# Kernel tuning notes

Hardware: AMD Instinct MI355X
Metric: run time of the kernel (lower is better)

## Reference

```python
import jax, jax.numpy as jnp
import numpy as np


def setup_inputs() -> dict:
    key = jax.random.key(0)
    k1, k2 = jax.random.split(key)
    N, D, K = 1048576, 128, 262144
    data = jax.random.normal(k1, (N, D), dtype=jnp.float32)
    # unique in-range indices (index depth 1 -> scatter rows of data)
    indices = jnp.arange(K, dtype=jnp.int64).reshape(K, 1)
    updates = jax.random.normal(k2, (K, D), dtype=jnp.float32)
    return {"data": data, "indices": indices, "updates": updates}


def reference(data, indices, updates):
    # ScatterND with reduction=1 (add): out = clone(data); out[idx] += updates
    # indices: [K, 1] -> row indices [K]; updates: [K, D]
    idx = indices[..., 0].astype(jnp.int32)
    # indices are unique, so .at[].add matches torch's gather-add-scatter exactly
    return data.at[idx].add(updates)
```

## Files before the change

### kernel.cpp

```cpp
#include <hip/hip_runtime.h>


__global__ void inv_init_kernel(int4* __restrict__ inv4, int n4) {
    int i = blockIdx.x * blockDim.x + threadIdx.x;
    if (i < n4) inv4[i] = make_int4(-1, -1, -1, -1);
}

__global__ void inv_scatter_kernel(const int* __restrict__ idx,
                                   int* __restrict__ inv, int K) {
    int k = blockIdx.x * blockDim.x + threadIdx.x;
    if (k < K) inv[idx[k]] = k;
}

__global__ void fused_scatter_add_kernel(const float4* __restrict__ data,
                                         const float4* __restrict__ upd,
                                         const int* __restrict__ inv,
                                         float4* __restrict__ out,
                                         int nvec, unsigned dvec) {
    int i = blockIdx.x * blockDim.x + threadIdx.x;
    if (i >= nvec) return;
    unsigned row  = (unsigned)i / dvec;
    unsigned lane = (unsigned)i - row * dvec;
    float4 v = data[i];
    int k = inv[row];
    if (k >= 0) {
        float4 u = upd[(long long)k * dvec + lane];
        v.x += u.x; v.y += u.y; v.z += u.z; v.w += u.w;
    }
    out[i] = v;
}

__global__ void copy_kernel(const float4* __restrict__ src,
                            float4* __restrict__ dst, int nvec) {
    int i = blockIdx.x * blockDim.x + threadIdx.x;
    if (i < nvec) dst[i] = src[i];
}

__global__ void rmw_add_kernel(const float4* __restrict__ upd,
                               const int* __restrict__ idx,
                               float4* __restrict__ out,
                               int kvec, unsigned dvec) {
    int i = blockIdx.x * blockDim.x + threadIdx.x;
    if (i >= kvec) return;
    unsigned k    = (unsigned)i / dvec;
    unsigned lane = (unsigned)i - k * dvec;
    long long off = (long long)idx[k] * dvec + lane;
    float4 u = upd[i];
    float4 v = out[off];
    v.x += u.x; v.y += u.y; v.z += u.z; v.w += u.w;
    out[off] = v;
}

extern "C" void kernel_launch(void* const* d_in, const int* in_sizes, int n_in,
                              void* d_out, int out_size, void* d_ws, size_t ws_size,
                              hipStream_t stream) {
    const float* data = (const float*)d_in[0];
    const int*   idx  = (const int*)d_in[1];
    const float* upd  = (const float*)d_in[2];
    float* out = (float*)d_out;

    const int K = in_sizes[1];
    const int D = in_sizes[2] / K;
    const int N = in_sizes[0] / D;
    const unsigned dvec = (unsigned)(D / 4);
    const int nvec = in_sizes[0] / 4;
    const int kvec = in_sizes[2] / 4;

    const int BS = 256;

    if (ws_size >= (size_t)N * sizeof(int)) {
        int* inv = (int*)d_ws;
        int n4 = N / 4;
        inv_init_kernel<<<(n4 + BS - 1) / BS, BS, 0, stream>>>((int4*)inv, n4);
        inv_scatter_kernel<<<(K + BS - 1) / BS, BS, 0, stream>>>(idx, inv, K);
        fused_scatter_add_kernel<<<(nvec + BS - 1) / BS, BS, 0, stream>>>(
            (const float4*)data, (const float4*)upd, inv, (float4*)out, nvec, dvec);
    } else {
        copy_kernel<<<(nvec + BS - 1) / BS, BS, 0, stream>>>(
            (const float4*)data, (float4*)out, nvec);
        rmw_add_kernel<<<(kvec + BS - 1) / BS, BS, 0, stream>>>(
            (const float4*)upd, idx, (float4*)out, kvec, dvec);
    }
}
```

Baseline: 894.4 us.

## Store inverse index map in output tail and use shift/mask indexing

The inverse row map now lives in the last rows of the output buffer instead of the workspace, so the fused gather-add path runs even when no workspace is provided. The fused kernel covers every row except those tail rows. The tail rows are then copied from the input, and a per-index kernel applies any updates that target them. Row and lane indexing use shift and mask when the vector width is a power of two. The change removes the fallback copy plus read-modify-write passes but adds two small extra launches and relies on the map being consumed before the tail is overwritten.

Result: no change. 898.3 us (+0.4%).

```diff
diff --git a/kernel.cpp b/kernel.cpp
--- a/kernel.cpp
+++ b/kernel.cpp
@@ -16,9 +16,28 @@
                                          const float4* __restrict__ upd,
                                          const int* __restrict__ inv,
                                          float4* __restrict__ out,
-                                         int nvec, unsigned dvec) {
+                                         int nvec_main, unsigned shift,
+                                         unsigned lanemask) {
     int i = blockIdx.x * blockDim.x + threadIdx.x;
-    if (i >= nvec) return;
+    if (i >= nvec_main) return;
+    unsigned row  = (unsigned)i >> shift;
+    unsigned lane = (unsigned)i & lanemask;
+    float4 v = data[i];
+    int k = inv[row];
+    if (k >= 0) {
+        float4 u = upd[((long long)k << shift) + lane];
+        v.x += u.x; v.y += u.y; v.z += u.z; v.w += u.w;
+    }
+    out[i] = v;
+}
+
+__global__ void fused_scatter_add_div_kernel(const float4* __restrict__ data,
+                                             const float4* __restrict__ upd,
+                                             const int* __restrict__ inv,
+                                             float4* __restrict__ out,
+                                             int nvec_main, unsigned dvec) {
+    int i = blockIdx.x * blockDim.x + threadIdx.x;
+    if (i >= nvec_main) return;
     unsigned row  = (unsigned)i / dvec;
     unsigned lane = (unsigned)i - row * dvec;
     float4 v = data[i];
@@ -36,19 +55,22 @@
     if (i < nvec) dst[i] = src[i];
 }
 
-__global__ void rmw_add_kernel(const float4* __restrict__ upd,
-                               const int* __restrict__ idx,
-                               float4* __restrict__ out,
-                               int kvec, unsigned dvec) {
-    int i = blockIdx.x * blockDim.x + threadIdx.x;
-    if (i >= kvec) return;
-    unsigned k    = (unsigned)i / dvec;
-    unsigned lane = (unsigned)i - k * dvec;
-    long long off = (long long)idx[k] * dvec + lane;
-    float4 u = upd[i];
-    float4 v = out[off];
-    v.x += u.x; v.y += u.y; v.z += u.z; v.w += u.w;
-    out[off] = v;
+__global__ void tail_rmw_kernel(const float4* __restrict__ upd,
+                                const int* __restrict__ idx,
+                                float4* __restrict__ out,
+                                int K, int row_lo, unsigned dvec) {
+    int k = blockIdx.x * blockDim.x + threadIdx.x;
+    if (k >= K) return;
+    int r = idx[k];
+    if (r < row_lo) return;
+    const float4* u = upd + (long long)k * dvec;
+    float4*       o = out + (long long)r * dvec;
+    for (unsigned j = 0; j < dvec; ++j) {
+        float4 v = o[j];
+        float4 uu = u[j];
+        v.x += uu.x; v.y += uu.y; v.z += uu.z; v.w += uu.w;
+        o[j] = v;
+    }
 }
 
 extern "C" void kernel_launch(void* const* d_in, const int* in_sizes, int n_in,
@@ -63,22 +85,38 @@
     const int D = in_sizes[2] / K;
     const int N = in_sizes[0] / D;
     const unsigned dvec = (unsigned)(D / 4);
-    const int nvec = in_sizes[0] / 4;
-    const int kvec = in_sizes[2] / 4;
 
     const int BS = 256;
 
-    if (ws_size >= (size_t)N * sizeof(int)) {
-        int* inv = (int*)d_ws;
-        int n4 = N / 4;
-        inv_init_kernel<<<(n4 + BS - 1) / BS, BS, 0, stream>>>((int4*)inv, n4);
-        inv_scatter_kernel<<<(K + BS - 1) / BS, BS, 0, stream>>>(idx, inv, K);
-        fused_scatter_add_kernel<<<(nvec + BS - 1) / BS, BS, 0, stream>>>(
-            (const float4*)data, (const float4*)upd, inv, (float4*)out, nvec, dvec);
+    const int T         = (N + D - 1) / D;
+    const int rows_main = N - T;
+    const int nvec_main = rows_main * (int)dvec;
+    const int tvec      = T * (int)dvec;
+
+    int* inv = (int*)out + (long long)rows_main * D;
+
+    int n4 = (N + 3) / 4;
+    inv_init_kernel<<<(n4 + BS - 1) / BS, BS, 0, stream>>>((int4*)inv, n4);
+
+    inv_scatter_kernel<<<(K + BS - 1) / BS, BS, 0, stream>>>(idx, inv, K);
+
+    bool pow2 = (dvec & (dvec - 1)) == 0;
+    if (pow2) {
+        unsigned shift = 0;
+        while ((1u << shift) < dvec) ++shift;
+        fused_scatter_add_kernel<<<(nvec_main + BS - 1) / BS, BS, 0, stream>>>(
+            (const float4*)data, (const float4*)upd, inv, (float4*)out,
+            nvec_main, shift, dvec - 1);
     } else {
-        copy_kernel<<<(nvec + BS - 1) / BS, BS, 0, stream>>>(
-            (const float4*)data, (float4*)out, nvec);
-        rmw_add_kernel<<<(kvec + BS - 1) / BS, BS, 0, stream>>>(
-            (const float4*)upd, idx, (float4*)out, kvec, dvec);
+        fused_scatter_add_div_kernel<<<(nvec_main + BS - 1) / BS, BS, 0, stream>>>(
+            (const float4*)data, (const float4*)upd, inv, (float4*)out,
+            nvec_main, dvec);
     }
+
+    copy_kernel<<<(tvec + BS - 1) / BS, BS, 0, stream>>>(
+        (const float4*)data + (long long)rows_main * dvec,
+        (float4*)out + (long long)rows_main * dvec, tvec);
+
+    tail_rmw_kernel<<<(K + BS - 1) / BS, BS, 0, stream>>>(
+        (const float4*)upd, idx, (float4*)out, K, rows_main, dvec);
 }
```
